# Kernel optimization log

Hardware: AMD Instinct MI355X
Metric: run time of the kernel (lower is better)

## Reference

```python
import jax, jax.numpy as jnp
from jax import lax
import numpy as np

B, H, Wd = 8, 56, 56
IC, IA = 8, 32        # input_num_capsule, input_num_atoms
OC, OA = 4, 16        # num_capsule, num_atoms
K_SZ, SCALE, ROUTINGS = 4, 2, 3


def setup_inputs() -> dict:
    key = jax.random.key(0)
    k1, k2, k3 = jax.random.split(key, 3)
    input_tensor = jax.random.normal(k1, (B, H, Wd, IC, IA), dtype=jnp.float32)
    # TF kernel layout for conv2d_transpose: [kh, kw, out_channels, in_channels]
    W = jax.random.normal(k2, (K_SZ, K_SZ, OC * OA, IA), dtype=jnp.float32) * 0.05
    b = jnp.full((1, 1, OC, OA), 0.1, dtype=jnp.float32)  # constant(0.1) init
    return {"input_tensor": input_tensor, "W": W, "b": b}


def _squash(v):
    # v / ||v|| * (||v||^2 / (1 + ||v||^2)), norm over last axis
    norm = jnp.linalg.norm(v, axis=-1, keepdims=True)
    norm_sq = norm * norm
    return v / norm * (norm_sq / (1.0 + norm_sq))


def reference(input_tensor, W, b):
    Bn, Hn, Wn, ICn, IAn = input_tensor.shape
    # [B,H,W,IC,IA] -> [B*IC, H, W, IA]
    x = jnp.transpose(input_tensor, (0, 3, 1, 2, 4)).reshape(Bn * ICn, Hn, Wn, IAn)
    # conv2d_transpose, stride=SCALE, SAME padding -> output spatial = in * SCALE
    out = lax.conv_transpose(
        x, W, (SCALE, SCALE), 'SAME',
        dimension_numbers=('NHWC', 'HWIO', 'NHWC'),
        transpose_kernel=True)  # matches TF conv2d_transpose with [kh,kw,out,in] kernel
    H2, W2 = out.shape[1], out.shape[2]
    votes = out.reshape(Bn, ICn, H2, W2, OC, OA)  # [B, IC, H2, W2, OC, OA]
    biases = jnp.broadcast_to(b, (H2, W2, OC, OA))

    logits = jnp.zeros((Bn, ICn, H2, W2, OC), dtype=votes.dtype)
    activation = None
    for _ in range(ROUTINGS):  # small fixed trip count
        route = jax.nn.softmax(logits, axis=-1)            # over output capsules
        preact = jnp.sum(route[..., None] * votes, axis=1) + biases  # sum over IC
        activation = _squash(preact)                        # [B, H2, W2, OC, OA]
        logits = logits + jnp.sum(votes * activation[:, None], axis=-1)
    return activation
```

## Files before the change

### kernel.cpp

```cpp
#include <hip/hip_runtime.h>
#include <hip/hip_bf16.h>


typedef __attribute__((ext_vector_type(8))) short bf16x8;
typedef __attribute__((ext_vector_type(4))) float f32x4;

static __device__ __forceinline__ bf16x8 cvt8(f32x4 a, f32x4 b) {
    union { unsigned u[4]; bf16x8 v; } r;
    asm("v_cvt_pk_bf16_f32 %0, %1, %2" : "=v"(r.u[0]) : "v"(a[0]), "v"(a[1]));
    asm("v_cvt_pk_bf16_f32 %0, %1, %2" : "=v"(r.u[1]) : "v"(a[2]), "v"(a[3]));
    asm("v_cvt_pk_bf16_f32 %0, %1, %2" : "=v"(r.u[2]) : "v"(b[0]), "v"(b[1]));
    asm("v_cvt_pk_bf16_f32 %0, %1, %2" : "=v"(r.u[3]) : "v"(b[2]), "v"(b[3]));
    return r.v;
}

static __device__ __forceinline__ __amdgpu_buffer_rsrc_t
make_srd(const void* base, int nrec) {
    uintptr_t p = (uintptr_t)base;
    unsigned lo = (unsigned)__builtin_amdgcn_readfirstlane((int)p);
    unsigned hi = (unsigned)__builtin_amdgcn_readfirstlane((int)(p >> 32));
    nrec = __builtin_amdgcn_readfirstlane(nrec);
    void* bp = (void*)(((uintptr_t)hi << 32) | lo);
    return __builtin_amdgcn_make_buffer_rsrc(bp, (short)0, nrec, 0x00020000);
}

static __device__ __forceinline__ void dpp_sum16_x4(float& a, float& b,
                                                    float& c, float& d) {
    asm("s_nop 1\n\t"
        "v_add_f32_dpp %0, %0, %0 quad_perm:[1,0,3,2] row_mask:0xf bank_mask:0xf\n\t"
        "v_add_f32_dpp %1, %1, %1 quad_perm:[1,0,3,2] row_mask:0xf bank_mask:0xf\n\t"
        "v_add_f32_dpp %2, %2, %2 quad_perm:[1,0,3,2] row_mask:0xf bank_mask:0xf\n\t"
        "v_add_f32_dpp %3, %3, %3 quad_perm:[1,0,3,2] row_mask:0xf bank_mask:0xf\n\t"
        "v_add_f32_dpp %0, %0, %0 quad_perm:[2,3,0,1] row_mask:0xf bank_mask:0xf\n\t"
        "v_add_f32_dpp %1, %1, %1 quad_perm:[2,3,0,1] row_mask:0xf bank_mask:0xf\n\t"
        "v_add_f32_dpp %2, %2, %2 quad_perm:[2,3,0,1] row_mask:0xf bank_mask:0xf\n\t"
        "v_add_f32_dpp %3, %3, %3 quad_perm:[2,3,0,1] row_mask:0xf bank_mask:0xf\n\t"
        "v_add_f32_dpp %0, %0, %0 row_half_mirror row_mask:0xf bank_mask:0xf\n\t"
        "v_add_f32_dpp %1, %1, %1 row_half_mirror row_mask:0xf bank_mask:0xf\n\t"
        "v_add_f32_dpp %2, %2, %2 row_half_mirror row_mask:0xf bank_mask:0xf\n\t"
        "v_add_f32_dpp %3, %3, %3 row_half_mirror row_mask:0xf bank_mask:0xf\n\t"
        "v_add_f32_dpp %0, %0, %0 row_mirror row_mask:0xf bank_mask:0xf\n\t"
        "v_add_f32_dpp %1, %1, %1 row_mirror row_mask:0xf bank_mask:0xf\n\t"
        "v_add_f32_dpp %2, %2, %2 row_mirror row_mask:0xf bank_mask:0xf\n\t"
        "v_add_f32_dpp %3, %3, %3 row_mirror row_mask:0xf bank_mask:0xf"
        : "+v"(a), "+v"(b), "+v"(c), "+v"(d));
}

static __device__ __forceinline__ void join16_x4(float& p0, float& p1,
                                                 float& p2, float& p3) {
    float q0 = p0, q1 = p1, q2 = p2, q3 = p3;
    asm("s_nop 1\n\t"
        "v_permlane16_swap_b32 %0, %4\n\t"
        "v_permlane16_swap_b32 %1, %5\n\t"
        "v_permlane16_swap_b32 %2, %6\n\t"
        "v_permlane16_swap_b32 %3, %7"
        : "+v"(p0), "+v"(p1), "+v"(p2), "+v"(p3),
          "+v"(q0), "+v"(q1), "+v"(q2), "+v"(q3));
    p0 += q0; p1 += q1; p2 += q2; p3 += q3;
}

static __device__ __forceinline__ void join32_x4(float& p0, float& p1,
                                                 float& p2, float& p3) {
    float q0 = p0, q1 = p1, q2 = p2, q3 = p3;
    asm("s_nop 1\n\t"
        "v_permlane32_swap_b32 %0, %4\n\t"
        "v_permlane32_swap_b32 %1, %5\n\t"
        "v_permlane32_swap_b32 %2, %6\n\t"
        "v_permlane32_swap_b32 %3, %7"
        : "+v"(p0), "+v"(p1), "+v"(p2), "+v"(p3),
          "+v"(q0), "+v"(q1), "+v"(q2), "+v"(q3));
    p0 += q0; p1 += q1; p2 += q2; p3 += q3;
}

__global__ __launch_bounds__(256, 5)
void caps_deconv_route(const float* __restrict__ in, const float* __restrict__ Wt,
                       const float* __restrict__ bia, float* __restrict__ out) {
    const int tid  = threadIdx.x;
    const int lane = tid & 63;
    const int wid  = tid >> 6;

    const int h    = blockIdx.x;
    const int b    = h & 7;
    const int r    = h >> 3;
    const int s80  = r >> 2;
    const int cls  = r & 3;
    const int py = cls >> 1, px = cls & 1;

    const int wv = s80*4 + wid;
    int start, np;
    if (wv < 288) { start = wv*5;       np = 5; }
    else          { start = 4*wv + 288; np = 4; }

    __shared__ uint4 wlds[1024];
    __shared__ float sw[4][192];
    for (int t = tid; t < 1024; t += 256) {
        const int s  = t >> 8;
        const int ko = (t >> 6) & 3;
        const int ch = t & 63;
        const int ky = 2*(s >> 1) + (py ^ 1);
        const int kx = 2*(s & 1)  + (px ^ 1);
        const float* wp = Wt + (((ky*4 + kx)*64 + ch)*32 + ko*8);
        const float4 w0 = *(const float4*)(wp);
        const float4 w1 = *(const float4*)(wp + 4);
        uint4 u;
        asm("v_cvt_pk_bf16_f32 %0, %1, %2" : "=v"(u.x) : "v"(w0.x), "v"(w0.y));
        asm("v_cvt_pk_bf16_f32 %0, %1, %2" : "=v"(u.y) : "v"(w0.z), "v"(w0.w));
        asm("v_cvt_pk_bf16_f32 %0, %1, %2" : "=v"(u.z) : "v"(w1.x), "v"(w1.y));
        asm("v_cvt_pk_bf16_f32 %0, %1, %2" : "=v"(u.w) : "v"(w1.z), "v"(w1.w));
        wlds[t] = u;
    }
    __syncthreads();

    const int col  = lane & 15;
    const int koct = lane >> 4;
    const int wbase = koct*64 + col;

    const int oa    = col;
    const int posl  = lane >> 5;
    const int ich   = (lane >> 4) & 1;
    const int a_pos = (lane >> 3) & 1;
    const int a_ic  = lane & 7;
    const int pi    = col;
    const int g     = koct;
    const int posT  = pi >> 3;

    float bias_v[4];
    #pragma unroll
    for (int oc = 0; oc < 4; ++oc) bias_v[oc] = bia[oc*16 + oa];

    float* swa = sw[wid];
    float* swr = sw[wid] + 128;

    const int laneoff = a_pos*1024 + a_ic*128 + koct*32;

    int p0v = start * 2;
    int y  = p0v / 56;
    int x0 = p0v - y*56;

    for (int i = 0; i < np; ++i) {
        const int iy0 = y + py, iy1 = y + py - 1;
        const __amdgpu_buffer_rsrc_t srd0 = make_srd(
            (const char*)in + (size_t)(b*56 + (iy0 < 0 ? 0 : (iy0 > 55 ? 55 : iy0))) * 57344,
            ((unsigned)iy0 < 56u) ? 57344 : 0);
        const __amdgpu_buffer_rsrc_t srd1 = make_srd(
            (const char*)in + (size_t)(b*56 + (iy1 < 0 ? 0 : (iy1 > 55 ? 55 : iy1))) * 57344,
            ((unsigned)iy1 < 56u) ? 57344 : 0);
        const int voff0 = (x0 + px) * 1024 + laneoff;
        const int voff1 = voff0 - 1024;

        f32x4 t0a = __builtin_bit_cast(f32x4, __builtin_amdgcn_raw_buffer_load_b128(srd0, voff0,      0, 0));
        f32x4 t0b = __builtin_bit_cast(f32x4, __builtin_amdgcn_raw_buffer_load_b128(srd0, voff0 + 16, 0, 0));
        f32x4 t1a = __builtin_bit_cast(f32x4, __builtin_amdgcn_raw_buffer_load_b128(srd0, voff1,      0, 0));
        f32x4 t1b = __builtin_bit_cast(f32x4, __builtin_amdgcn_raw_buffer_load_b128(srd0, voff1 + 16, 0, 0));
        f32x4 t2a = __builtin_bit_cast(f32x4, __builtin_amdgcn_raw_buffer_load_b128(srd1, voff0,      0, 0));
        f32x4 t2b = __builtin_bit_cast(f32x4, __builtin_amdgcn_raw_buffer_load_b128(srd1, voff0 + 16, 0, 0));
        f32x4 t3a = __builtin_bit_cast(f32x4, __builtin_amdgcn_raw_buffer_load_b128(srd1, voff1,      0, 0));
        f32x4 t3b = __builtin_bit_cast(f32x4, __builtin_amdgcn_raw_buffer_load_b128(srd1, voff1 + 16, 0, 0));

        bf16x8 af0 = cvt8(t0a, t0b);
        bf16x8 af1 = cvt8(t1a, t1b);
        bf16x8 af2 = cvt8(t2a, t2b);
        bf16x8 af3 = cvt8(t3a, t3b);

        f32x4 acc[4], accT[4];
        __builtin_amdgcn_s_setprio(1);
        #pragma unroll
        for (int nt = 0; nt < 4; ++nt) {
            bf16x8 wf = __builtin_bit_cast(bf16x8, wlds[wbase + nt*16]);
            acc[nt]  = __builtin_amdgcn_mfma_f32_16x16x32_bf16(
                af0, wf, (f32x4){0.f,0.f,0.f,0.f}, 0, 0, 0);
            accT[nt] = __builtin_amdgcn_mfma_f32_16x16x32_bf16(
                wf, af0, (f32x4){0.f,0.f,0.f,0.f}, 0, 0, 0);
        }
        #pragma unroll
        for (int nt = 0; nt < 4; ++nt) {
            bf16x8 wf = __builtin_bit_cast(bf16x8, wlds[wbase + 256 + nt*16]);
            acc[nt]  = __builtin_amdgcn_mfma_f32_16x16x32_bf16(af1, wf, acc[nt], 0, 0, 0);
            accT[nt] = __builtin_amdgcn_mfma_f32_16x16x32_bf16(wf, af1, accT[nt], 0, 0, 0);
        }
        #pragma unroll
        for (int nt = 0; nt < 4; ++nt) {
            bf16x8 wf = __builtin_bit_cast(bf16x8, wlds[wbase + 512 + nt*16]);
            acc[nt]  = __builtin_amdgcn_mfma_f32_16x16x32_bf16(af2, wf, acc[nt], 0, 0, 0);
            accT[nt] = __builtin_amdgcn_mfma_f32_16x16x32_bf16(wf, af2, accT[nt], 0, 0, 0);
        }
        #pragma unroll
        for (int nt = 0; nt < 4; ++nt) {
            bf16x8 wf = __builtin_bit_cast(bf16x8, wlds[wbase + 768 + nt*16]);
            acc[nt]  = __builtin_amdgcn_mfma_f32_16x16x32_bf16(af3, wf, acc[nt], 0, 0, 0);
            accT[nt] = __builtin_amdgcn_mfma_f32_16x16x32_bf16(wf, af3, accT[nt], 0, 0, 0);
        }
        __builtin_amdgcn_s_setprio(0);

        float p[4], sq[4], act[4];
        #pragma unroll
        for (int oc = 0; oc < 4; ++oc)
            p[oc] = (acc[oc][0] + acc[oc][1]) + (acc[oc][2] + acc[oc][3]);
        join16_x4(p[0], p[1], p[2], p[3]);
        #pragma unroll
        for (int oc = 0; oc < 4; ++oc) {
            p[oc] = fmaf(0.25f, p[oc], bias_v[oc]);
            sq[oc] = p[oc] * p[oc];
        }
        dpp_sum16_x4(sq[0], sq[1], sq[2], sq[3]);
        #pragma unroll
        for (int oc = 0; oc < 4; ++oc)
            act[oc] = p[oc] * (__builtin_amdgcn_sqrtf(sq[oc]) * __builtin_amdgcn_rcpf(1.f + sq[oc]));

        if (ich == 0) {
            #pragma unroll
            for (int oc = 0; oc < 4; ++oc) swa[posl*64 + oc*16 + oa] = act[oc];
        }
        asm volatile("s_waitcnt lgkmcnt(0)" ::: "memory");
        float logit[4];
        #pragma unroll
        for (int oc = 0; oc < 4; ++oc) {
            float4 at = *(const float4*)&swa[posT*64 + oc*16 + g*4];
            float t = accT[oc][0]*at.x;
            t = fmaf(accT[oc][1], at.y, t);
            t = fmaf(accT[oc][2], at.z, t);
            t = fmaf(accT[oc][3], at.w, t);
            logit[oc] = t;
        }
        join16_x4(logit[0], logit[1], logit[2], logit[3]);
        join32_x4(logit[0], logit[1], logit[2], logit[3]);

        #pragma unroll
        for (int it = 1; it < 3; ++it) {
            float e0 = __expf(logit[0]), e1 = __expf(logit[1]);
            float e2 = __expf(logit[2]), e3 = __expf(logit[3]);
            float inv = __builtin_amdgcn_rcpf((e0 + e1) + (e2 + e3));
            if (lane < 16) {
                float4 rt = make_float4(e0*inv, e1*inv, e2*inv, e3*inv);
                *(float4*)&swr[pi*4] = rt;
            }
            asm volatile("s_waitcnt lgkmcnt(0)" ::: "memory");
            const int rb = (posl*8 + ich*4) * 4;
            float4 rq0 = *(const float4*)&swr[rb];
            float4 rq1 = *(const float4*)&swr[rb + 4];
            float4 rq2 = *(const float4*)&swr[rb + 8];
            float4 rq3 = *(const float4*)&swr[rb + 12];

            p[0] = fmaf(rq3.x, acc[0][3], fmaf(rq2.x, acc[0][2],
                   fmaf(rq1.x, acc[0][1], rq0.x*acc[0][0])));
            p[1] = fmaf(rq3.y, acc[1][3], fmaf(rq2.y, acc[1][2],
                   fmaf(rq1.y, acc[1][1], rq0.y*acc[1][0])));
            p[2] = fmaf(rq3.z, acc[2][3], fmaf(rq2.z, acc[2][2],
                   fmaf(rq1.z, acc[2][1], rq0.z*acc[2][0])));
            p[3] = fmaf(rq3.w, acc[3][3], fmaf(rq2.w, acc[3][2],
                   fmaf(rq1.w, acc[3][1], rq0.w*acc[3][0])));
            join16_x4(p[0], p[1], p[2], p[3]);
            #pragma unroll
            for (int oc = 0; oc < 4; ++oc) {
                p[oc] += bias_v[oc];
                sq[oc] = p[oc] * p[oc];
            }
            dpp_sum16_x4(sq[0], sq[1], sq[2], sq[3]);
            #pragma unroll
            for (int oc = 0; oc < 4; ++oc)
                act[oc] = p[oc] * (__builtin_amdgcn_sqrtf(sq[oc]) * __builtin_amdgcn_rcpf(1.f + sq[oc]));

            if (it == 1) {
                if (ich == 0) {
                    #pragma unroll
                    for (int oc = 0; oc < 4; ++oc) swa[posl*64 + oc*16 + oa] = act[oc];
                }
                asm volatile("s_waitcnt lgkmcnt(0)" ::: "memory");
                float upd[4];
                #pragma unroll
                for (int oc = 0; oc < 4; ++oc) {
                    float4 at = *(const float4*)&swa[posT*64 + oc*16 + g*4];
                    float t = accT[oc][0]*at.x;
                    t = fmaf(accT[oc][1], at.y, t);
                    t = fmaf(accT[oc][2], at.z, t);
                    t = fmaf(accT[oc][3], at.w, t);
                    upd[oc] = t;
                }
                join16_x4(upd[0], upd[1], upd[2], upd[3]);
                join32_x4(upd[0], upd[1], upd[2], upd[3]);
                #pragma unroll
                for (int oc = 0; oc < 4; ++oc) logit[oc] += upd[oc];
            }
        }

        if (ich == 0) {
            const int oy = 2*y + py;
            const int ox = 2*(x0 + posl) + px;
            float* op = out + ((((size_t)b*112 + oy)*112 + ox)*64 + oa);
            #pragma unroll
            for (int oc = 0; oc < 4; ++oc) op[oc*16] = act[oc];
        }

        x0 += 2;
        if (x0 >= 56) { x0 -= 56; ++y; }
    }
}

extern "C" void kernel_launch(void* const* d_in, const int* in_sizes, int n_in,
                              void* d_out, int out_size, void* d_ws, size_t ws_size,
                              hipStream_t stream) {
    const float* in  = (const float*)d_in[0];
    const float* Wt  = (const float*)d_in[1];
    const float* bia = (const float*)d_in[2];
    float* out = (float*)d_out;
    hipLaunchKernelGGL(caps_deconv_route, dim3(2560), dim3(256), 0, stream,
                       in, Wt, bia, out);
}
```

Baseline: 64.78 us.

## Prefetch next position's input loads and rebalance grid to fewer blocks

Software-pipelines the per-position global loads: the next position's eight buffer loads are issued right after converting the current inputs, so memory latency overlaps with the MFMA and routing work. At the same time the grid shrinks from 2560 to 2048 blocks, with each wave covering 6–7 positions instead of 4–5, and launch bounds drop to 4 blocks per CU. The extra live registers for prefetched data may reduce occupancy. The coarser work split trades parallelism for fewer block-setup costs, such as the per-block weight staging into LDS.

```diff
diff --git a/kernel.cpp b/kernel.cpp
--- a/kernel.cpp
+++ b/kernel.cpp
@@ -72,7 +72,7 @@
     p0 += q0; p1 += q1; p2 += q2; p3 += q3;
 }
 
-__global__ __launch_bounds__(256, 5)
+__global__ __launch_bounds__(256, 4)
 void caps_deconv_route(const float* __restrict__ in, const float* __restrict__ Wt,
                        const float* __restrict__ bia, float* __restrict__ out) {
     const int tid  = threadIdx.x;
@@ -82,14 +82,14 @@
     const int h    = blockIdx.x;
     const int b    = h & 7;
     const int r    = h >> 3;
-    const int s80  = r >> 2;
+    const int s64  = r >> 2;
     const int cls  = r & 3;
     const int py = cls >> 1, px = cls & 1;
 
-    const int wv = s80*4 + wid;
+    const int wv = s64*4 + wid;
     int start, np;
-    if (wv < 288) { start = wv*5;       np = 5; }
-    else          { start = 4*wv + 288; np = 4; }
+    if (wv < 32) { start = wv*7;      np = 7; }
+    else         { start = wv*6 + 32; np = 6; }
 
     __shared__ uint4 wlds[1024];
     __shared__ float sw[4][192];
@@ -137,30 +137,44 @@
     int y  = p0v / 56;
     int x0 = p0v - y*56;
 
-    for (int i = 0; i < np; ++i) {
-        const int iy0 = y + py, iy1 = y + py - 1;
-        const __amdgpu_buffer_rsrc_t srd0 = make_srd(
+    f32x4 t0a, t0b, t1a, t1b, t2a, t2b, t3a, t3b;
+
+    auto issue_loads = [&](int yy, int xx) {
+        const int iy0 = yy + py, iy1 = iy0 - 1;
+        const __amdgpu_buffer_rsrc_t s0 = make_srd(
             (const char*)in + (size_t)(b*56 + (iy0 < 0 ? 0 : (iy0 > 55 ? 55 : iy0))) * 57344,
             ((unsigned)iy0 < 56u) ? 57344 : 0);
-        const __amdgpu_buffer_rsrc_t srd1 = make_srd(
+        const __amdgpu_buffer_rsrc_t s1 = make_srd(
             (const char*)in + (size_t)(b*56 + (iy1 < 0 ? 0 : (iy1 > 55 ? 55 : iy1))) * 57344,
             ((unsigned)iy1 < 56u) ? 57344 : 0);
-        const int voff0 = (x0 + px) * 1024 + laneoff;
-        const int voff1 = voff0 - 1024;
-
-        f32x4 t0a = __builtin_bit_cast(f32x4, __builtin_amdgcn_raw_buffer_load_b128(srd0, voff0,      0, 0));
-        f32x4 t0b = __builtin_bit_cast(f32x4, __builtin_amdgcn_raw_buffer_load_b128(srd0, voff0 + 16, 0, 0));
-        f32x4 t1a = __builtin_bit_cast(f32x4, __builtin_amdgcn_raw_buffer_load_b128(srd0, voff1,      0, 0));
-        f32x4 t1b = __builtin_bit_cast(f32x4, __builtin_amdgcn_raw_buffer_load_b128(srd0, voff1 + 16, 0, 0));
-        f32x4 t2a = __builtin_bit_cast(f32x4, __builtin_amdgcn_raw_buffer_load_b128(srd1, voff0,      0, 0));
-        f32x4 t2b = __builtin_bit_cast(f32x4, __builtin_amdgcn_raw_buffer_load_b128(srd1, voff0 + 16, 0, 0));
-        f32x4 t3a = __builtin_bit_cast(f32x4, __builtin_amdgcn_raw_buffer_load_b128(srd1, voff1,      0, 0));
-        f32x4 t3b = __builtin_bit_cast(f32x4, __builtin_amdgcn_raw_buffer_load_b128(srd1, voff1 + 16, 0, 0));
+        const int v0 = (xx + px) * 1024 + laneoff;
+        const int v1 = v0 - 1024;
+        t0a = __builtin_bit_cast(f32x4, __builtin_amdgcn_raw_buffer_load_b128(s0, v0,      0, 0));
+        t0b = __builtin_bit_cast(f32x4, __builtin_amdgcn_raw_buffer_load_b128(s0, v0 + 16, 0, 0));
+        t1a = __builtin_bit_cast(f32x4, __builtin_amdgcn_raw_buffer_load_b128(s0, v1,      0, 0));
+        t1b = __builtin_bit_cast(f32x4, __builtin_amdgcn_raw_buffer_load_b128(s0, v1 + 16, 0, 0));
+        t2a = __builtin_bit_cast(f32x4, __builtin_amdgcn_raw_buffer_load_b128(s1, v0,      0, 0));
+        t2b = __builtin_bit_cast(f32x4, __builtin_amdgcn_raw_buffer_load_b128(s1, v0 + 16, 0, 0));
+        t3a = __builtin_bit_cast(f32x4, __builtin_amdgcn_raw_buffer_load_b128(s1, v1,      0, 0));
+        t3b = __builtin_bit_cast(f32x4, __builtin_amdgcn_raw_buffer_load_b128(s1, v1 + 16, 0, 0));
+    };
+
+    issue_loads(y, x0);
+
+    for (int i = 0; i < np; ++i) {
+        const int oy = 2*y + py;
+        const int ox = 2*(x0 + posl) + px;
 
         bf16x8 af0 = cvt8(t0a, t0b);
         bf16x8 af1 = cvt8(t1a, t1b);
         bf16x8 af2 = cvt8(t2a, t2b);
         bf16x8 af3 = cvt8(t3a, t3b);
+
+        if (i + 1 < np) {
+            x0 += 2;
+            if (x0 >= 56) { x0 -= 56; ++y; }
+            issue_loads(y, x0);
+        }
 
         f32x4 acc[4], accT[4];
         __builtin_amdgcn_s_setprio(1);
@@ -284,15 +298,10 @@
         }
 
         if (ich == 0) {
-            const int oy = 2*y + py;
-            const int ox = 2*(x0 + posl) + px;
             float* op = out + ((((size_t)b*112 + oy)*112 + ox)*64 + oa);
             #pragma unroll
             for (int oc = 0; oc < 4; ++oc) op[oc*16] = act[oc];
         }
-
-        x0 += 2;
-        if (x0 >= 56) { x0 -= 56; ++y; }
     }
 }
 
@@ -303,6 +312,6 @@
     const float* Wt  = (const float*)d_in[1];
     const float* bia = (const float*)d_in[2];
     float* out = (float*)d_out;
-    hipLaunchKernelGGL(caps_deconv_route, dim3(2560), dim3(256), 0, stream,
+    hipLaunchKernelGGL(caps_deconv_route, dim3(2048), dim3(256), 0, stream,
                        in, Wt, bia, out);
 }
```

Measured after the change: 65.84 us. About the same (+1.6%).

## Drop duplicate MFMA layout and LDS exchange; route entirely in transposed layout

Applied to the files above, without the earlier changes.

The votes used to be computed twice with MFMA, once per operand order (acc and accT). Now only the transposed accumulator is kept, which halves the MFMA work. Routing sums, squash and softmax weights are computed directly in that layout using DPP reductions over 8 lanes plus permlane joins, so the per-wave LDS scratch buffers and their waitcnt round trips are gone. The output is written as float4 stores, at the cost of more VALU shuffle work per lane and more registers.

```diff
diff --git a/kernel.cpp b/kernel.cpp
--- a/kernel.cpp
+++ b/kernel.cpp
@@ -24,8 +24,8 @@
     return __builtin_amdgcn_make_buffer_rsrc(bp, (short)0, nrec, 0x00020000);
 }
 
-static __device__ __forceinline__ void dpp_sum16_x4(float& a, float& b,
-                                                    float& c, float& d) {
+static __device__ __forceinline__ void dpp_sum8_x4(float& a, float& b,
+                                                   float& c, float& d) {
     asm("s_nop 1\n\t"
         "v_add_f32_dpp %0, %0, %0 quad_perm:[1,0,3,2] row_mask:0xf bank_mask:0xf\n\t"
         "v_add_f32_dpp %1, %1, %1 quad_perm:[1,0,3,2] row_mask:0xf bank_mask:0xf\n\t"
@@ -38,11 +38,7 @@
         "v_add_f32_dpp %0, %0, %0 row_half_mirror row_mask:0xf bank_mask:0xf\n\t"
         "v_add_f32_dpp %1, %1, %1 row_half_mirror row_mask:0xf bank_mask:0xf\n\t"
         "v_add_f32_dpp %2, %2, %2 row_half_mirror row_mask:0xf bank_mask:0xf\n\t"
-        "v_add_f32_dpp %3, %3, %3 row_half_mirror row_mask:0xf bank_mask:0xf\n\t"
-        "v_add_f32_dpp %0, %0, %0 row_mirror row_mask:0xf bank_mask:0xf\n\t"
-        "v_add_f32_dpp %1, %1, %1 row_mirror row_mask:0xf bank_mask:0xf\n\t"
-        "v_add_f32_dpp %2, %2, %2 row_mirror row_mask:0xf bank_mask:0xf\n\t"
-        "v_add_f32_dpp %3, %3, %3 row_mirror row_mask:0xf bank_mask:0xf"
+        "v_add_f32_dpp %3, %3, %3 row_half_mirror row_mask:0xf bank_mask:0xf"
         : "+v"(a), "+v"(b), "+v"(c), "+v"(d));
 }
 
@@ -92,7 +88,6 @@
     else          { start = 4*wv + 288; np = 4; }
 
     __shared__ uint4 wlds[1024];
-    __shared__ float sw[4][192];
     for (int t = tid; t < 1024; t += 256) {
         const int s  = t >> 8;
         const int ko = (t >> 6) & 3;
@@ -112,26 +107,19 @@
     __syncthreads();
 
     const int col  = lane & 15;
-    const int koct = lane >> 4;
-    const int wbase = koct*64 + col;
-
-    const int oa    = col;
-    const int posl  = lane >> 5;
-    const int ich   = (lane >> 4) & 1;
+    const int g    = lane >> 4;
+    const int wbase = g*64 + col;
+    const int p_   = col >> 3;
+    const int icl  = col & 7;
+
     const int a_pos = (lane >> 3) & 1;
     const int a_ic  = lane & 7;
-    const int pi    = col;
-    const int g     = koct;
-    const int posT  = pi >> 3;
-
-    float bias_v[4];
+
+    float4 biasT[4];
     #pragma unroll
-    for (int oc = 0; oc < 4; ++oc) bias_v[oc] = bia[oc*16 + oa];
-
-    float* swa = sw[wid];
-    float* swr = sw[wid] + 128;
-
-    const int laneoff = a_pos*1024 + a_ic*128 + koct*32;
+    for (int oc = 0; oc < 4; ++oc) biasT[oc] = *(const float4*)&bia[oc*16 + g*4];
+
+    const int laneoff = a_pos*1024 + a_ic*128 + g*32;
 
     int p0v = start * 2;
     int y  = p0v / 56;
@@ -162,64 +150,65 @@
         bf16x8 af2 = cvt8(t2a, t2b);
         bf16x8 af3 = cvt8(t3a, t3b);
 
-        f32x4 acc[4], accT[4];
+        f32x4 accT[4];
         __builtin_amdgcn_s_setprio(1);
         #pragma unroll
         for (int nt = 0; nt < 4; ++nt) {
             bf16x8 wf = __builtin_bit_cast(bf16x8, wlds[wbase + nt*16]);
-            acc[nt]  = __builtin_amdgcn_mfma_f32_16x16x32_bf16(
-                af0, wf, (f32x4){0.f,0.f,0.f,0.f}, 0, 0, 0);
             accT[nt] = __builtin_amdgcn_mfma_f32_16x16x32_bf16(
                 wf, af0, (f32x4){0.f,0.f,0.f,0.f}, 0, 0, 0);
         }
         #pragma unroll
         for (int nt = 0; nt < 4; ++nt) {
             bf16x8 wf = __builtin_bit_cast(bf16x8, wlds[wbase + 256 + nt*16]);
-            acc[nt]  = __builtin_amdgcn_mfma_f32_16x16x32_bf16(af1, wf, acc[nt], 0, 0, 0);
             accT[nt] = __builtin_amdgcn_mfma_f32_16x16x32_bf16(wf, af1, accT[nt], 0, 0, 0);
         }
         #pragma unroll
         for (int nt = 0; nt < 4; ++nt) {
             bf16x8 wf = __builtin_bit_cast(bf16x8, wlds[wbase + 512 + nt*16]);
-            acc[nt]  = __builtin_amdgcn_mfma_f32_16x16x32_bf16(af2, wf, acc[nt], 0, 0, 0);
             accT[nt] = __builtin_amdgcn_mfma_f32_16x16x32_bf16(wf, af2, accT[nt], 0, 0, 0);
         }
         #pragma unroll
         for (int nt = 0; nt < 4; ++nt) {
             bf16x8 wf = __builtin_bit_cast(bf16x8, wlds[wbase + 768 + nt*16]);
-            acc[nt]  = __builtin_amdgcn_mfma_f32_16x16x32_bf16(af3, wf, acc[nt], 0, 0, 0);
             accT[nt] = __builtin_amdgcn_mfma_f32_16x16x32_bf16(wf, af3, accT[nt], 0, 0, 0);
         }
         __builtin_amdgcn_s_setprio(0);
 
-        float p[4], sq[4], act[4];
+        float S[4][4], actT[4][4], sqv[4], logit[4];
+
         #pragma unroll
         for (int oc = 0; oc < 4; ++oc)
-            p[oc] = (acc[oc][0] + acc[oc][1]) + (acc[oc][2] + acc[oc][3]);
-        join16_x4(p[0], p[1], p[2], p[3]);
+            #pragma unroll
+            for (int rr = 0; rr < 4; ++rr) S[oc][rr] = accT[oc][rr];
+        #pragma unroll
+        for (int oc = 0; oc < 4; ++oc)
+            dpp_sum8_x4(S[oc][0], S[oc][1], S[oc][2], S[oc][3]);
         #pragma unroll
         for (int oc = 0; oc < 4; ++oc) {
-            p[oc] = fmaf(0.25f, p[oc], bias_v[oc]);
-            sq[oc] = p[oc] * p[oc];
-        }
-        dpp_sum16_x4(sq[0], sq[1], sq[2], sq[3]);
-        #pragma unroll
-        for (int oc = 0; oc < 4; ++oc)
-            act[oc] = p[oc] * (__builtin_amdgcn_sqrtf(sq[oc]) * __builtin_amdgcn_rcpf(1.f + sq[oc]));
-
-        if (ich == 0) {
-            #pragma unroll
-            for (int oc = 0; oc < 4; ++oc) swa[posl*64 + oc*16 + oa] = act[oc];
-        }
-        asm volatile("s_waitcnt lgkmcnt(0)" ::: "memory");
-        float logit[4];
+            #pragma unroll
+            for (int rr = 0; rr < 4; ++rr)
+                S[oc][rr] = fmaf(0.25f, S[oc][rr], biasT[oc][rr]);
+            float t = S[oc][0]*S[oc][0];
+            t = fmaf(S[oc][1], S[oc][1], t);
+            t = fmaf(S[oc][2], S[oc][2], t);
+            t = fmaf(S[oc][3], S[oc][3], t);
+            sqv[oc] = t;
+        }
+        join16_x4(sqv[0], sqv[1], sqv[2], sqv[3]);
+        join32_x4(sqv[0], sqv[1], sqv[2], sqv[3]);
         #pragma unroll
         for (int oc = 0; oc < 4; ++oc) {
-            float4 at = *(const float4*)&swa[posT*64 + oc*16 + g*4];
-            float t = accT[oc][0]*at.x;
-            t = fmaf(accT[oc][1], at.y, t);
-            t = fmaf(accT[oc][2], at.z, t);
-            t = fmaf(accT[oc][3], at.w, t);
+            float fac = __builtin_amdgcn_sqrtf(sqv[oc]) * __builtin_amdgcn_rcpf(1.f + sqv[oc]);
+            #pragma unroll
+            for (int rr = 0; rr < 4; ++rr) actT[oc][rr] = S[oc][rr] * fac;
+        }
+        #pragma unroll
+        for (int oc = 0; oc < 4; ++oc) {
+            float t = accT[oc][0]*actT[oc][0];
+            t = fmaf(accT[oc][1], actT[oc][1], t);
+            t = fmaf(accT[oc][2], actT[oc][2], t);
+            t = fmaf(accT[oc][3], actT[oc][3], t);
             logit[oc] = t;
         }
         join16_x4(logit[0], logit[1], logit[2], logit[3]);
@@ -230,50 +219,40 @@
             float e0 = __expf(logit[0]), e1 = __expf(logit[1]);
             float e2 = __expf(logit[2]), e3 = __expf(logit[3]);
             float inv = __builtin_amdgcn_rcpf((e0 + e1) + (e2 + e3));
-            if (lane < 16) {
-                float4 rt = make_float4(e0*inv, e1*inv, e2*inv, e3*inv);
-                *(float4*)&swr[pi*4] = rt;
-            }
-            asm volatile("s_waitcnt lgkmcnt(0)" ::: "memory");
-            const int rb = (posl*8 + ich*4) * 4;
-            float4 rq0 = *(const float4*)&swr[rb];
-            float4 rq1 = *(const float4*)&swr[rb + 4];
-            float4 rq2 = *(const float4*)&swr[rb + 8];
-            float4 rq3 = *(const float4*)&swr[rb + 12];
-
-            p[0] = fmaf(rq3.x, acc[0][3], fmaf(rq2.x, acc[0][2],
-                   fmaf(rq1.x, acc[0][1], rq0.x*acc[0][0])));
-            p[1] = fmaf(rq3.y, acc[1][3], fmaf(rq2.y, acc[1][2],
-                   fmaf(rq1.y, acc[1][1], rq0.y*acc[1][0])));
-            p[2] = fmaf(rq3.z, acc[2][3], fmaf(rq2.z, acc[2][2],
-                   fmaf(rq1.z, acc[2][1], rq0.z*acc[2][0])));
-            p[3] = fmaf(rq3.w, acc[3][3], fmaf(rq2.w, acc[3][2],
-                   fmaf(rq1.w, acc[3][1], rq0.w*acc[3][0])));
-            join16_x4(p[0], p[1], p[2], p[3]);
+            float rt[4] = {e0*inv, e1*inv, e2*inv, e3*inv};
+            #pragma unroll
+            for (int oc = 0; oc < 4; ++oc)
+                #pragma unroll
+                for (int rr = 0; rr < 4; ++rr) S[oc][rr] = rt[oc]*accT[oc][rr];
+            #pragma unroll
+            for (int oc = 0; oc < 4; ++oc)
+                dpp_sum8_x4(S[oc][0], S[oc][1], S[oc][2], S[oc][3]);
             #pragma unroll
             for (int oc = 0; oc < 4; ++oc) {
-                p[oc] += bias_v[oc];
-                sq[oc] = p[oc] * p[oc];
-            }
-            dpp_sum16_x4(sq[0], sq[1], sq[2], sq[3]);
-            #pragma unroll
-            for (int oc = 0; oc < 4; ++oc)
-                act[oc] = p[oc] * (__builtin_amdgcn_sqrtf(sq[oc]) * __builtin_amdgcn_rcpf(1.f + sq[oc]));
-
+                #pragma unroll
+                for (int rr = 0; rr < 4; ++rr) S[oc][rr] += biasT[oc][rr];
+                float t = S[oc][0]*S[oc][0];
+                t = fmaf(S[oc][1], S[oc][1], t);
+                t = fmaf(S[oc][2], S[oc][2], t);
+                t = fmaf(S[oc][3], S[oc][3], t);
+                sqv[oc] = t;
+            }
+            join16_x4(sqv[0], sqv[1], sqv[2], sqv[3]);
+            join32_x4(sqv[0], sqv[1], sqv[2], sqv[3]);
+            #pragma unroll
+            for (int oc = 0; oc < 4; ++oc) {
+                float fac = __builtin_amdgcn_sqrtf(sqv[oc]) * __builtin_amdgcn_rcpf(1.f + sqv[oc]);
+                #pragma unroll
+                for (int rr = 0; rr < 4; ++rr) actT[oc][rr] = S[oc][rr] * fac;
+            }
             if (it == 1) {
-                if (ich == 0) {
-                    #pragma unroll
-                    for (int oc = 0; oc < 4; ++oc) swa[posl*64 + oc*16 + oa] = act[oc];
-                }
-                asm volatile("s_waitcnt lgkmcnt(0)" ::: "memory");
                 float upd[4];
                 #pragma unroll
                 for (int oc = 0; oc < 4; ++oc) {
-                    float4 at = *(const float4*)&swa[posT*64 + oc*16 + g*4];
-                    float t = accT[oc][0]*at.x;
-                    t = fmaf(accT[oc][1], at.y, t);
-                    t = fmaf(accT[oc][2], at.z, t);
-                    t = fmaf(accT[oc][3], at.w, t);
+                    float t = accT[oc][0]*actT[oc][0];
+                    t = fmaf(accT[oc][1], actT[oc][1], t);
+                    t = fmaf(accT[oc][2], actT[oc][2], t);
+                    t = fmaf(accT[oc][3], actT[oc][3], t);
                     upd[oc] = t;
                 }
                 join16_x4(upd[0], upd[1], upd[2], upd[3]);
@@ -283,12 +262,16 @@
             }
         }
 
-        if (ich == 0) {
+        if (icl == 0) {
             const int oy = 2*y + py;
-            const int ox = 2*(x0 + posl) + px;
-            float* op = out + ((((size_t)b*112 + oy)*112 + ox)*64 + oa);
-            #pragma unroll
-            for (int oc = 0; oc < 4; ++oc) op[oc*16] = act[oc];
+            const int ox = 2*(x0 + p_) + px;
+            float* op = out + ((((size_t)b*112 + oy)*112 + ox)*64 + g*4);
+            #pragma unroll
+            for (int oc = 0; oc < 4; ++oc) {
+                float4 v = make_float4(actT[oc][0], actT[oc][1],
+                                       actT[oc][2], actT[oc][3]);
+                *(float4*)(op + oc*16) = v;
+            }
         }
 
         x0 += 2;
```

After: 75.39 us. 16.4% more time.
